# Optimization experiments

Hardware: AMD Instinct MI355X
Metric: run time of the kernel (lower is better)

Reference implementation:

```python
import jax, jax.numpy as jnp
import numpy as np

D_STATE = 8
D_CONV = 4
DT_RANK = 8
THRESHOLD = 0.5
KPOOL = 3
PAD = (KPOOL - 1) // 2
EPS = 1e-5


def _rmsnorm(x, w):
    return x * jax.lax.rsqrt(jnp.mean(x * x, axis=-1, keepdims=True) + EPS) * w


def _dw_causal_conv(x, w, b):
    # x: (L, T, C), w: (C, 1, K) depthwise causal conv along T
    xt = jnp.transpose(x, (0, 2, 1))  # (L, C, T)
    y = jax.lax.conv_general_dilated(
        xt, w, window_strides=(1,), padding=[(D_CONV - 1, 0)],
        dimension_numbers=('NCH', 'OIH', 'NCH'), feature_group_count=xt.shape[1])
    return jnp.transpose(y, (0, 2, 1)) + b


def _selective_scan(x, delta, A, B, Cm, D):
    # x, delta: (L,T,d); A: (d,n); B, Cm: (L,T,n); D: (d,)
    dA = jnp.exp(delta[..., None] * A)                        # (L,T,d,n)
    dBx = (delta * x)[..., None] * B[:, :, None, :]           # (L,T,d,n)
    def combine(a, b):
        a1, b1 = a
        a2, b2 = b
        return (a2 * a1, a2 * b1 + b2)
    _, h = jax.lax.associative_scan(combine, (dA, dBx), axis=1)
    y = jnp.einsum('ltdn,ltn->ltd', h, Cm)
    return y + x * D


def _mamba_block(x, in_proj, conv_w, conv_b, x_proj_w, dt_proj_w, dt_proj_b,
                 A_log_f, A_log_b, D_f, D_b, out_proj_w, rms_w):
    # single-depth bidirectional (bimamba-v2 style) block, expand=1, residual + RMSNorm
    res = x
    xn = _rmsnorm(x, rms_w)
    xz = xn @ in_proj                       # (L,T,2C)
    xi, z = jnp.split(xz, 2, axis=-1)
    xi = jax.nn.silu(_dw_causal_conv(xi, conv_w, conv_b))
    dbl = xi @ x_proj_w                     # (L,T,dt_rank+2*d_state)
    dt = dbl[..., :DT_RANK]
    Bm = dbl[..., DT_RANK:DT_RANK + D_STATE]
    Cm = dbl[..., DT_RANK + D_STATE:]
    delta = jax.nn.softplus(dt @ dt_proj_w + dt_proj_b)
    A_f = -jnp.exp(A_log_f)
    A_b = -jnp.exp(A_log_b)
    flip = lambda a: a[:, ::-1]
    y_f = _selective_scan(xi, delta, A_f, Bm, Cm, D_f)
    y_b = flip(_selective_scan(flip(xi), flip(delta), A_b, flip(Bm), flip(Cm), D_b))
    y = 0.5 * (y_f + y_b) * jax.nn.silu(z)  # if_devide_out -> average two directions
    return res + y @ out_proj_w


def reference(feats, in_proj, conv_w, conv_b, x_proj_w, dt_proj_w, dt_proj_b,
              A_log_f, A_log_b, D_f, D_b, out_proj_w, rms_w, mlp_w, mlp_b,
              record_len):
    N, C, H, W = feats.shape
    T = H * W
    rec = np.asarray(record_len)  # static ragged group sizes
    ends = np.cumsum(rec)
    starts = ends - rec
    masks = []
    for s0, L in zip(starts.tolist(), rec.tolist()):
        g = feats[s0:s0 + L]                       # (L,C,H,W)
        if L > 1:
            x = g.reshape(L, C, T).transpose(0, 2, 1)  # l c h w -> l (h w) c
            feat = _mamba_block(x, in_proj, conv_w, conv_b, x_proj_w, dt_proj_w,
                                dt_proj_b, A_log_f, A_log_b, D_f, D_b,
                                out_proj_w, rms_w)
            score = jax.nn.sigmoid(feat @ mlp_w + mlp_b)   # (L,T,1)
            ego = jnp.ones((1, T, 1), feats.dtype)
            bs = jnp.concatenate([ego, score[1:]], axis=0)
        else:
            bs = jnp.ones((1, T, 1), feats.dtype)
        bs = bs.transpose(0, 2, 1).reshape(L, 1, H, W)     # l (h w) c -> l c h w
        masks.append(jnp.where(bs > THRESHOLD, 1.0, 0.0).astype(feats.dtype))
    mask = jnp.concatenate(masks, axis=0)                  # (N,1,H,W)
    pooled = jax.lax.reduce_window(
        mask, -jnp.inf, jax.lax.max,
        window_dimensions=(1, 1, KPOOL, KPOOL), window_strides=(1, 1, 1, 1),
        padding=[(0, 0), (0, 0), (PAD, PAD), (PAD, PAD)])
    return pooled


def setup_inputs():
    key = jax.random.key(0)
    ks = jax.random.split(key, 8)
    C, H, W = 128, 96, 96
    record_len = np.array([2, 3, 1, 2, 4], dtype=np.int64)
    N = int(record_len.sum())
    s = 0.05
    A_log = jnp.log(jnp.broadcast_to(
        jnp.arange(1, D_STATE + 1, dtype=jnp.float32), (C, D_STATE)))
    return {
        'feats': jax.random.normal(ks[0], (N, C, H, W), jnp.float32),
        'in_proj': jax.random.normal(ks[1], (C, 2 * C), jnp.float32) * s,
        'conv_w': jax.random.normal(ks[2], (C, 1, D_CONV), jnp.float32) * s,
        'conv_b': jnp.zeros((C,), jnp.float32),
        'x_proj_w': jax.random.normal(ks[3], (C, DT_RANK + 2 * D_STATE), jnp.float32) * s,
        'dt_proj_w': jax.random.normal(ks[4], (DT_RANK, C), jnp.float32) * s,
        'dt_proj_b': jnp.full((C,), 0.1, jnp.float32),
        'A_log_f': A_log,
        'A_log_b': A_log,
        'D_f': jnp.ones((C,), jnp.float32),
        'D_b': jnp.ones((C,), jnp.float32),
        'out_proj_w': jax.random.normal(ks[5], (C, C), jnp.float32) * s,
        'rms_w': jnp.ones((C,), jnp.float32),
        'mlp_w': jax.random.normal(ks[6], (C, 1), jnp.float32) * s,
        'mlp_b': jnp.zeros((1,), jnp.float32),
        'record_len': jnp.asarray(record_len),
    }
```

## Files before the change

kernel.cpp:

```cpp
#include <hip/hip_runtime.h>
#include <cstdint>
#include <cstddef>

#define C_CH 128
#define T_TOK 9216
#define H_IMG 96
#define W_IMG 96
#define NSTATE 8

#define CHUNK 64
#define RHALO 32
#define REGION (CHUNK + 2 * RHALO)

__device__ __forceinline__ float siluf_dev(float x) {
  return x / (1.0f + expf(-x));
}

__device__ __forceinline__ float fast_silu(float x) {
  return __fdividef(x, 1.0f + __expf(-x));
}

__global__ __launch_bounds__(128) void k0_setup(
    const int* __restrict__ rec, int n_groups, int N,
    const float* __restrict__ out_proj_w, const float* __restrict__ mlp_w,
    float* __restrict__ vvec, int* __restrict__ slot)
{
  const int tid = threadIdx.x;
  if (tid == 0) {
    int f = 0, sl = 0;
    for (int g = 0; g < n_groups; ++g) {
      const int L = rec[g];
      slot[f] = -1;
      for (int i = 1; i < L; ++i) slot[f + i] = sl++;
      f += L;
    }
  }
  if (tid < C_CH) {
    float acc = 0.0f;
    for (int j = 0; j < C_CH; ++j) acc += out_proj_w[tid * C_CH + j] * mlp_w[j];
    vvec[tid] = acc;
  }
}

__global__ __launch_bounds__(256, 4) void k1_gemm(
    const float* __restrict__ feats, const float* __restrict__ in_proj,
    const float* __restrict__ rms_w, const float* __restrict__ mlp_w,
    const float* __restrict__ mlp_b, const float* __restrict__ vvec,
    const int* __restrict__ slot,
    float* __restrict__ xipre, float* __restrict__ wbuf,
    float* __restrict__ logit)
{
  __shared__ float Asm[C_CH * 64];
  __shared__ float redA[256], redB[256], irS[64];
  const int f = blockIdx.y;
  const int s = slot[f];
  if (s < 0) return;
  const int m0 = blockIdx.x * 64;
  const int tid = threadIdx.x;

  {
    const int c0 = tid >> 4;
    const int tq = (tid & 15) * 4;
    const float* src = feats + (size_t)f * C_CH * T_TOK + m0 + tq;
    #pragma unroll
    for (int i = 0; i < 8; ++i) {
      const int c = c0 + i * 16;
      const float4 x4 = *(const float4*)(src + (size_t)c * T_TOK);
      *(float4*)&Asm[c * 64 + tq] = x4;
    }
  }
  __syncthreads();
  {
    const int t = tid & 63;
    const int q = tid >> 6;
    float ssum = 0.0f, rm = 0.0f;
    for (int cc = q * 32; cc < q * 32 + 32; ++cc) {
      const float val = Asm[cc * 64 + t];
      ssum += val * val;
      rm += val * mlp_w[cc];
    }
    redA[tid] = ssum; redB[tid] = rm;
  }
  __syncthreads();
  if (tid < 64) {
    const int t = tid;
    const float ssum = redA[t] + redA[t + 64] + redA[t + 128] + redA[t + 192];
    const float rm   = redB[t] + redB[t + 64] + redB[t + 128] + redB[t + 192];
    const float ir = 1.0f / sqrtf(ssum * (1.0f / C_CH) + 1e-5f);
    logit[(size_t)s * T_TOK + m0 + t] = rm + mlp_b[0];
    irS[t] = ir;
  }
  __syncthreads();
  {
    const int t = tid & 63;
    const int q = tid >> 6;
    const float ir = irS[t];
    for (int cc = q * 32; cc < q * 32 + 32; ++cc)
      Asm[cc * 64 + t] = (Asm[cc * 64 + t] * ir) * rms_w[cc];
  }
  __syncthreads();

  const int ti = tid >> 4;
  const int tc = tid & 15;
  for (int chunk = 0; chunk < 4; ++chunk) {
    const int n0 = chunk * 64;
    const float* bp = in_proj + n0 + tc * 4;
    float acc[4][4];
    #pragma unroll
    for (int i = 0; i < 4; ++i)
      #pragma unroll
      for (int j = 0; j < 4; ++j) acc[i][j] = 0.0f;

    float4 bA = *(const float4*)(bp);
    float4 aA = *(const float4*)&Asm[ti * 4];
    #pragma unroll 2
    for (int k = 0; k < C_CH; k += 2) {
      const int kB = k + 1;
      const int kN = (k + 2 < C_CH) ? (k + 2) : (C_CH - 1);
      const float4 bB = *(const float4*)(bp + (size_t)kB * 256);
      const float4 aB = *(const float4*)&Asm[kB * 64 + ti * 4];
      acc[0][0] += aA.x * bA.x; acc[0][1] += aA.x * bA.y; acc[0][2] += aA.x * bA.z; acc[0][3] += aA.x * bA.w;
      acc[1][0] += aA.y * bA.x; acc[1][1] += aA.y * bA.y; acc[1][2] += aA.y * bA.z; acc[1][3] += aA.y * bA.w;
      acc[2][0] += aA.z * bA.x; acc[2][1] += aA.z * bA.y; acc[2][2] += aA.z * bA.z; acc[2][3] += aA.z * bA.w;
      acc[3][0] += aA.w * bA.x; acc[3][1] += aA.w * bA.y; acc[3][2] += aA.w * bA.z; acc[3][3] += aA.w * bA.w;
      const float4 bN = *(const float4*)(bp + (size_t)kN * 256);
      const float4 aN = *(const float4*)&Asm[kN * 64 + ti * 4];
      acc[0][0] += aB.x * bB.x; acc[0][1] += aB.x * bB.y; acc[0][2] += aB.x * bB.z; acc[0][3] += aB.x * bB.w;
      acc[1][0] += aB.y * bB.x; acc[1][1] += aB.y * bB.y; acc[1][2] += aB.y * bB.z; acc[1][3] += aB.y * bB.w;
      acc[2][0] += aB.z * bB.x; acc[2][1] += aB.z * bB.y; acc[2][2] += aB.z * bB.z; acc[2][3] += aB.z * bB.w;
      acc[3][0] += aB.w * bB.x; acc[3][1] += aB.w * bB.y; acc[3][2] += aB.w * bB.z; acc[3][3] += aB.w * bB.w;
      bA = bN; aA = aN;
    }

    if (chunk < 2) {
      const int cb = n0 + tc * 4;
      #pragma unroll
      for (int i = 0; i < 4; ++i) {
        const int t = m0 + ti * 4 + i;
        float4 o; o.x = acc[i][0]; o.y = acc[i][1]; o.z = acc[i][2]; o.w = acc[i][3];
        *(float4*)&xipre[((size_t)s * T_TOK + t) * C_CH + cb] = o;
      }
    } else {
      const int zc = (chunk - 2) * 64 + tc * 4;
      const float4 v4 = *(const float4*)&vvec[zc];
      #pragma unroll
      for (int i = 0; i < 4; ++i) {
        const int t = m0 + ti * 4 + i;
        float4 o;
        o.x = 0.5f * siluf_dev(acc[i][0]) * v4.x;
        o.y = 0.5f * siluf_dev(acc[i][1]) * v4.y;
        o.z = 0.5f * siluf_dev(acc[i][2]) * v4.z;
        o.w = 0.5f * siluf_dev(acc[i][3]) * v4.w;
        *(float4*)&wbuf[((size_t)s * T_TOK + t) * C_CH + zc] = o;
      }
    }
  }
}

__global__ __launch_bounds__(256, 4) void k2_convproj(
    const float* __restrict__ xipre,
    const float* __restrict__ conv_w, const float* __restrict__ conv_b,
    const float* __restrict__ x_proj_w,
    const float* __restrict__ dt_proj_w, const float* __restrict__ dt_proj_b,
    const int* __restrict__ slot,
    float* __restrict__ xd_g, float* __restrict__ bc_g)
{
  __shared__ float xibuf[64 * 129];
  __shared__ float dtb[64 * 8];
  const int f = blockIdx.y;
  const int s = slot[f];
  if (s < 0) return;
  const int m0 = blockIdx.x * 64;
  const int tid = threadIdx.x;
  const int c = tid & 127;
  const int half = tid >> 7;
  const size_t rowbase = (size_t)s * T_TOK;
  const float4 cw = *(const float4*)(conv_w + c * 4);
  const float cb = conv_b[c];

  auto ldx = [&](int t) -> float {
    return (t >= 0) ? xipre[(rowbase + t) * C_CH + c] : 0.0f;
  };

  {
    const int t0 = m0 + half * 32;
    float xm1 = ldx(t0 - 1), xm2 = ldx(t0 - 2), xm3 = ldx(t0 - 3);
    #pragma unroll
    for (int i = 0; i < 32; ++i) {
      const float cur = ldx(t0 + i);
      const float sum = cw.x * xm3 + cw.y * xm2 + cw.z * xm1 + cw.w * cur + cb;
      xibuf[(half * 32 + i) * 129 + c] = fast_silu(sum);
      xm3 = xm2; xm2 = xm1; xm1 = cur;
    }
  }
  __syncthreads();
  {
    const int q6 = __builtin_amdgcn_readfirstlane(tid >> 6) * 6;
    const int tok = tid & 63;
    float acc[6] = {0, 0, 0, 0, 0, 0};
    for (int cc = 0; cc < C_CH; ++cc) {
      const float xv = xibuf[tok * 129 + cc];
      #pragma unroll
      for (int jj = 0; jj < 6; ++jj)
        acc[jj] += xv * x_proj_w[cc * 24 + q6 + jj];
    }
    #pragma unroll
    for (int jj = 0; jj < 6; ++jj) {
      const int o = q6 + jj;
      if (o < 8) dtb[tok * 8 + o] = acc[jj];
      else       bc_g[(rowbase + m0 + tok) * 16 + (o - 8)] = acc[jj];
    }
  }
  __syncthreads();
  {
    float dw[8];
    #pragma unroll
    for (int r = 0; r < 8; ++r) dw[r] = dt_proj_w[r * C_CH + c];
    const float bias = dt_proj_b[c];
    for (int i = 0; i < 32; ++i) {
      const int tok = half * 32 + i;
      const float4 d0 = *(const float4*)&dtb[tok * 8];
      const float4 d1 = *(const float4*)&dtb[tok * 8 + 4];
      float pre = bias;
      pre += d0.x * dw[0] + d0.y * dw[1] + d0.z * dw[2] + d0.w * dw[3];
      pre += d1.x * dw[4] + d1.y * dw[5] + d1.z * dw[6] + d1.w * dw[7];
      const float dlt = fmaxf(pre, 0.0f) + __logf(1.0f + __expf(-fabsf(pre)));
      float2 xd;
      xd.x = xibuf[tok * 129 + c];
      xd.y = dlt;
      *(float2*)&xd_g[(rowbase + m0 + tok) * (2 * C_CH) + c * 2] = xd;
    }
  }
}

__global__ __launch_bounds__(256, 4) void k3_scan(
    const float* __restrict__ xd_g, const float* __restrict__ wbuf,
    const float* __restrict__ bc_g,
    const float* __restrict__ A_log_f, const float* __restrict__ A_log_b,
    const float* __restrict__ D_f, const float* __restrict__ D_b,
    const int* __restrict__ slot, float* __restrict__ logit)
{
  __shared__ float bc[REGION * 16];
  const int f = blockIdx.y;
  const int s = slot[f];
  if (s < 0) return;
  const int c0 = blockIdx.x * CHUNK;
  const int r0 = c0 - RHALO;
  const int tid = threadIdx.x;
  const int c = tid & 127;
  const int half = tid >> 7;
  const size_t rowbase = (size_t)s * T_TOK;

  {
    const long grow = ((long)rowbase + r0) * 16;
    const int lo  = (r0 < 0) ? (-r0) * 4 : 0;
    const int hi  = (r0 + REGION > T_TOK) ? (T_TOK - r0) * 4 : REGION * 4;
    #pragma unroll
    for (int i = 0; i < 2; ++i) {
      const int idx = tid + i * 256;
      if (idx >= lo && idx < hi)
        *(float4*)&bc[idx * 4] = *(const float4*)&bc_g[grow + (long)idx * 4];
    }
  }
  __syncthreads();

  float Ac[8];
  const float* Alog = half ? A_log_b : A_log_f;
  #pragma unroll
  for (int n = 0; n < NSTATE; ++n) Ac[n] = -expf(Alog[c * NSTATE + n]);
  const float Dd = half ? D_b[c] : D_f[c];
  float h[8] = {0, 0, 0, 0, 0, 0, 0, 0};

  const float a0 = Ac[0];
  int okl = 1;
  #pragma unroll
  for (int n = 1; n < NSTATE; ++n)
    okl &= (fabsf(Ac[n] - (float)(n + 1) * a0) <= 1e-4f * fabsf(Ac[n])) ? 1 : 0;
  const bool fastA = (__all(okl) != 0);

  auto decay8 = [&](float dlt, float* dA) {
    if (fastA) {
      const float e1 = __expf(dlt * a0);
      const float e2 = e1 * e1, e3 = e2 * e1, e4 = e2 * e2;
      dA[0] = e1; dA[1] = e2; dA[2] = e3; dA[3] = e4;
      dA[4] = e4 * e1; dA[5] = e4 * e2; dA[6] = e4 * e3; dA[7] = e4 * e4;
    } else {
      #pragma unroll
      for (int n = 0; n < NSTATE; ++n) dA[n] = __expf(dlt * Ac[n]);
    }
  };

  if (half == 0) {
    const int tb = (r0 < 0) ? 0 : r0;
    const int outg0 = (c0 - tb) >> 3;
    const int ng = (c0 + CHUNK - tb) >> 3;
    for (int g = 0; g < ng; ++g) {
      const int t0 = tb + g * 8;
      const bool out = (g >= outg0);
      float xg[8], dg[8], wg[8];
      #pragma unroll
      for (int j = 0; j < 8; ++j) {
        const size_t r = rowbase + t0 + j;
        const float2 xd = *(const float2*)&xd_g[r * (2 * C_CH) + c * 2];
        xg[j] = xd.x;
        dg[j] = xd.y;
        wg[j] = out ? wbuf[r * C_CH + c] : 0.0f;
      }
      #pragma unroll
      for (int j = 0; j < 8; ++j) {
        const int t = t0 + j;
        const int p = t - r0;
        const float dlt = dg[j];
        const float xiv = xg[j];
        const float u = dlt * xiv;
        const float4 b0 = *(const float4*)&bc[p * 16];
        const float4 b1 = *(const float4*)&bc[p * 16 + 4];
        float dA[8];
        decay8(dlt, dA);
        h[0] = dA[0] * h[0] + u * b0.x;
        h[1] = dA[1] * h[1] + u * b0.y;
        h[2] = dA[2] * h[2] + u * b0.z;
        h[3] = dA[3] * h[3] + u * b0.w;
        h[4] = dA[4] * h[4] + u * b1.x;
        h[5] = dA[5] * h[5] + u * b1.y;
        h[6] = dA[6] * h[6] + u * b1.z;
        h[7] = dA[7] * h[7] + u * b1.w;
        if (out) {
          const float4 cc0 = *(const float4*)&bc[p * 16 + 8];
          const float4 cc1 = *(const float4*)&bc[p * 16 + 12];
          float y = xiv * Dd;
          y += h[0] * cc0.x + h[1] * cc0.y + h[2] * cc0.z + h[3] * cc0.w;
          y += h[4] * cc1.x + h[5] * cc1.y + h[6] * cc1.z + h[7] * cc1.w;
          float contrib = y * wg[j];
          contrib += __shfl_xor(contrib, 1);
          contrib += __shfl_xor(contrib, 2);
          contrib += __shfl_xor(contrib, 4);
          contrib += __shfl_xor(contrib, 8);
          contrib += __shfl_xor(contrib, 16);
          contrib += __shfl_xor(contrib, 32);
          if ((tid & 63) == 0) atomicAdd(&logit[rowbase + t], contrib);
        }
      }
    }
  } else {
    const int te2e = r0 + REGION;
    const int te2 = (te2e > T_TOK) ? T_TOK : te2e;
    const int outg0 = (te2 - (c0 + CHUNK)) >> 3;
    const int ng = (te2 - c0) >> 3;
    for (int g = 0; g < ng; ++g) {
      const int t0 = te2 - 1 - g * 8;
      const bool out = (g >= outg0);
      float xg[8], dg[8], wg[8];
      #pragma unroll
      for (int j = 0; j < 8; ++j) {
        const size_t r = rowbase + t0 - j;
        const float2 xd = *(const float2*)&xd_g[r * (2 * C_CH) + c * 2];
        xg[j] = xd.x;
        dg[j] = xd.y;
        wg[j] = out ? wbuf[r * C_CH + c] : 0.0f;
      }
      #pragma unroll
      for (int j = 0; j < 8; ++j) {
        const int t = t0 - j;
        const int p = t - r0;
        const float dlt = dg[j];
        const float xiv = xg[j];
        const float u = dlt * xiv;
        const float4 b0 = *(const float4*)&bc[p * 16];
        const float4 b1 = *(const float4*)&bc[p * 16 + 4];
        float dA[8];
        decay8(dlt, dA);
        h[0] = dA[0] * h[0] + u * b0.x;
        h[1] = dA[1] * h[1] + u * b0.y;
        h[2] = dA[2] * h[2] + u * b0.z;
        h[3] = dA[3] * h[3] + u * b0.w;
        h[4] = dA[4] * h[4] + u * b1.x;
        h[5] = dA[5] * h[5] + u * b1.y;
        h[6] = dA[6] * h[6] + u * b1.z;
        h[7] = dA[7] * h[7] + u * b1.w;
        if (out) {
          const float4 cc0 = *(const float4*)&bc[p * 16 + 8];
          const float4 cc1 = *(const float4*)&bc[p * 16 + 12];
          float y = xiv * Dd;
          y += h[0] * cc0.x + h[1] * cc0.y + h[2] * cc0.z + h[3] * cc0.w;
          y += h[4] * cc1.x + h[5] * cc1.y + h[6] * cc1.z + h[7] * cc1.w;
          float contrib = y * wg[j];
          contrib += __shfl_xor(contrib, 1);
          contrib += __shfl_xor(contrib, 2);
          contrib += __shfl_xor(contrib, 4);
          contrib += __shfl_xor(contrib, 8);
          contrib += __shfl_xor(contrib, 16);
          contrib += __shfl_xor(contrib, 32);
          if ((tid & 63) == 0) atomicAdd(&logit[rowbase + t], contrib);
        }
      }
    }
  }
}

__global__ __launch_bounds__(128) void k4_pool(
    const float* __restrict__ logit, const int* __restrict__ slot,
    float* __restrict__ out)
{
  const int w = threadIdx.x;
  if (w >= W_IMG) return;
  const int hh = blockIdx.x;
  const int f = blockIdx.y;
  const int s = slot[f];
  float m = 0.0f;
  if (s < 0) {
    m = 1.0f;
  } else {
    for (int dh = -1; dh <= 1; ++dh) {
      const int h2 = hh + dh;
      if (h2 < 0 || h2 >= H_IMG) continue;
      for (int dw = -1; dw <= 1; ++dw) {
        const int w2 = w + dw;
        if (w2 < 0 || w2 >= W_IMG) continue;
        if (logit[(size_t)s * T_TOK + h2 * W_IMG + w2] > 0.0f) m = 1.0f;
      }
    }
  }
  out[(size_t)f * T_TOK + hh * W_IMG + w] = m;
}

extern "C" void kernel_launch(void* const* d_in, const int* in_sizes, int n_in,
                              void* d_out, int out_size, void* d_ws, size_t ws_size,
                              hipStream_t stream) {
  const float* feats      = (const float*)d_in[0];
  const float* in_proj    = (const float*)d_in[1];
  const float* conv_w     = (const float*)d_in[2];
  const float* conv_b     = (const float*)d_in[3];
  const float* x_proj_w   = (const float*)d_in[4];
  const float* dt_proj_w  = (const float*)d_in[5];
  const float* dt_proj_b  = (const float*)d_in[6];
  const float* A_log_f    = (const float*)d_in[7];
  const float* A_log_b    = (const float*)d_in[8];
  const float* D_f        = (const float*)d_in[9];
  const float* D_b        = (const float*)d_in[10];
  const float* out_proj_w = (const float*)d_in[11];
  const float* rms_w      = (const float*)d_in[12];
  const float* mlp_w      = (const float*)d_in[13];
  const float* mlp_b      = (const float*)d_in[14];
  const int*   rec        = (const int*)d_in[15];

  const int N = in_sizes[0] / (C_CH * T_TOK);
  const int n_groups = in_sizes[15];
  int S = N - n_groups;
  if (S < 1) S = 1;

  char* p = (char*)d_ws;
  float* vvec  = (float*)p; p += 1024;
  int*   slot  = (int*)p;   p += ((N * 4 + 255) / 256) * 256;
  float* logit = (float*)p; p += (size_t)S * T_TOK * 4;
  float* xipre = (float*)p; p += (size_t)S * T_TOK * C_CH * 4;
  float* wA    = (float*)p; p += (size_t)S * T_TOK * C_CH * 4;
  float* xd    = (float*)p; p += (size_t)S * T_TOK * (2 * C_CH) * 4;
  float* bcg   = (float*)p; p += (size_t)S * T_TOK * 16 * 4;
  (void)ws_size; (void)n_in; (void)out_size;

  k0_setup<<<1, 128, 0, stream>>>(rec, n_groups, N, out_proj_w, mlp_w, vvec, slot);
  k1_gemm<<<dim3(T_TOK / 64, N), 256, 0, stream>>>(
      feats, in_proj, rms_w, mlp_w, mlp_b, vvec, slot, xipre, wA, logit);
  k2_convproj<<<dim3(T_TOK / 64, N), 256, 0, stream>>>(
      xipre, conv_w, conv_b, x_proj_w, dt_proj_w, dt_proj_b, slot,
      xd, bcg);
  k3_scan<<<dim3(T_TOK / CHUNK, N), 256, 0, stream>>>(
      xd, wA, bcg, A_log_f, A_log_b, D_f, D_b, slot, logit);
  k4_pool<<<dim3(H_IMG, N), 128, 0, stream>>>(logit, slot, (float*)d_out);
}
```

Measured before the change: 328.0 us.

## Fuse in-projection GEMM with causal conv and x-projection, recomputing halo tokens

Merges the in_proj GEMM kernel and the conv/x_proj kernel into one kernel, so the pre-conv xi activations stay in shared memory and no longer go through a global round trip. The three causal-conv halo tokens before each 64-token tile are loaded, RMS-normalised and projected again inside each block. This removes one launch and the xipre buffer traffic. In exchange it adds redundant halo compute and a larger shared footprint (padded stride, reused buffer), which may lower occupancy. The GEMM inner loop is also simplified from manual double-buffering to a plain unroll-8 loop.

```diff
diff --git a/kernel.cpp b/kernel.cpp
--- a/kernel.cpp
+++ b/kernel.cpp
@@ -11,6 +11,10 @@
 #define CHUNK 64
 #define RHALO 32
 #define REGION (CHUNK + 2 * RHALO)
+
+#define ASTRIDE 68
+#define XSTRIDE 129
+#define AU_FLOATS 8704
 
 __device__ __forceinline__ float siluf_dev(float x) {
   return x / (1.0f + expf(-x));
@@ -42,164 +46,198 @@
   }
 }
 
-__global__ __launch_bounds__(256, 4) void k1_gemm(
+__global__ __launch_bounds__(256, 4) void k12_gemmproj(
     const float* __restrict__ feats, const float* __restrict__ in_proj,
     const float* __restrict__ rms_w, const float* __restrict__ mlp_w,
     const float* __restrict__ mlp_b, const float* __restrict__ vvec,
-    const int* __restrict__ slot,
-    float* __restrict__ xipre, float* __restrict__ wbuf,
-    float* __restrict__ logit)
-{
-  __shared__ float Asm[C_CH * 64];
-  __shared__ float redA[256], redB[256], irS[64];
-  const int f = blockIdx.y;
-  const int s = slot[f];
-  if (s < 0) return;
-  const int m0 = blockIdx.x * 64;
-  const int tid = threadIdx.x;
-
-  {
-    const int c0 = tid >> 4;
-    const int tq = (tid & 15) * 4;
-    const float* src = feats + (size_t)f * C_CH * T_TOK + m0 + tq;
-    #pragma unroll
-    for (int i = 0; i < 8; ++i) {
-      const int c = c0 + i * 16;
-      const float4 x4 = *(const float4*)(src + (size_t)c * T_TOK);
-      *(float4*)&Asm[c * 64 + tq] = x4;
-    }
-  }
-  __syncthreads();
-  {
-    const int t = tid & 63;
-    const int q = tid >> 6;
-    float ssum = 0.0f, rm = 0.0f;
-    for (int cc = q * 32; cc < q * 32 + 32; ++cc) {
-      const float val = Asm[cc * 64 + t];
-      ssum += val * val;
-      rm += val * mlp_w[cc];
-    }
-    redA[tid] = ssum; redB[tid] = rm;
-  }
-  __syncthreads();
-  if (tid < 64) {
-    const int t = tid;
-    const float ssum = redA[t] + redA[t + 64] + redA[t + 128] + redA[t + 192];
-    const float rm   = redB[t] + redB[t + 64] + redB[t + 128] + redB[t + 192];
-    const float ir = 1.0f / sqrtf(ssum * (1.0f / C_CH) + 1e-5f);
-    logit[(size_t)s * T_TOK + m0 + t] = rm + mlp_b[0];
-    irS[t] = ir;
-  }
-  __syncthreads();
-  {
-    const int t = tid & 63;
-    const int q = tid >> 6;
-    const float ir = irS[t];
-    for (int cc = q * 32; cc < q * 32 + 32; ++cc)
-      Asm[cc * 64 + t] = (Asm[cc * 64 + t] * ir) * rms_w[cc];
-  }
-  __syncthreads();
-
-  const int ti = tid >> 4;
-  const int tc = tid & 15;
-  for (int chunk = 0; chunk < 4; ++chunk) {
-    const int n0 = chunk * 64;
-    const float* bp = in_proj + n0 + tc * 4;
-    float acc[4][4];
-    #pragma unroll
-    for (int i = 0; i < 4; ++i)
-      #pragma unroll
-      for (int j = 0; j < 4; ++j) acc[i][j] = 0.0f;
-
-    float4 bA = *(const float4*)(bp);
-    float4 aA = *(const float4*)&Asm[ti * 4];
-    #pragma unroll 2
-    for (int k = 0; k < C_CH; k += 2) {
-      const int kB = k + 1;
-      const int kN = (k + 2 < C_CH) ? (k + 2) : (C_CH - 1);
-      const float4 bB = *(const float4*)(bp + (size_t)kB * 256);
-      const float4 aB = *(const float4*)&Asm[kB * 64 + ti * 4];
-      acc[0][0] += aA.x * bA.x; acc[0][1] += aA.x * bA.y; acc[0][2] += aA.x * bA.z; acc[0][3] += aA.x * bA.w;
-      acc[1][0] += aA.y * bA.x; acc[1][1] += aA.y * bA.y; acc[1][2] += aA.y * bA.z; acc[1][3] += aA.y * bA.w;
-      acc[2][0] += aA.z * bA.x; acc[2][1] += aA.z * bA.y; acc[2][2] += aA.z * bA.z; acc[2][3] += aA.z * bA.w;
-      acc[3][0] += aA.w * bA.x; acc[3][1] += aA.w * bA.y; acc[3][2] += aA.w * bA.z; acc[3][3] += aA.w * bA.w;
-      const float4 bN = *(const float4*)(bp + (size_t)kN * 256);
-      const float4 aN = *(const float4*)&Asm[kN * 64 + ti * 4];
-      acc[0][0] += aB.x * bB.x; acc[0][1] += aB.x * bB.y; acc[0][2] += aB.x * bB.z; acc[0][3] += aB.x * bB.w;
-      acc[1][0] += aB.y * bB.x; acc[1][1] += aB.y * bB.y; acc[1][2] += aB.y * bB.z; acc[1][3] += aB.y * bB.w;
-      acc[2][0] += aB.z * bB.x; acc[2][1] += aB.z * bB.y; acc[2][2] += aB.z * bB.z; acc[2][3] += aB.z * bB.w;
-      acc[3][0] += aB.w * bB.x; acc[3][1] += aB.w * bB.y; acc[3][2] += aB.w * bB.z; acc[3][3] += aB.w * bB.w;
-      bA = bN; aA = aN;
-    }
-
-    if (chunk < 2) {
-      const int cb = n0 + tc * 4;
-      #pragma unroll
-      for (int i = 0; i < 4; ++i) {
-        const int t = m0 + ti * 4 + i;
-        float4 o; o.x = acc[i][0]; o.y = acc[i][1]; o.z = acc[i][2]; o.w = acc[i][3];
-        *(float4*)&xipre[((size_t)s * T_TOK + t) * C_CH + cb] = o;
-      }
-    } else {
-      const int zc = (chunk - 2) * 64 + tc * 4;
-      const float4 v4 = *(const float4*)&vvec[zc];
-      #pragma unroll
-      for (int i = 0; i < 4; ++i) {
-        const int t = m0 + ti * 4 + i;
-        float4 o;
-        o.x = 0.5f * siluf_dev(acc[i][0]) * v4.x;
-        o.y = 0.5f * siluf_dev(acc[i][1]) * v4.y;
-        o.z = 0.5f * siluf_dev(acc[i][2]) * v4.z;
-        o.w = 0.5f * siluf_dev(acc[i][3]) * v4.w;
-        *(float4*)&wbuf[((size_t)s * T_TOK + t) * C_CH + zc] = o;
-      }
-    }
-  }
-}
-
-__global__ __launch_bounds__(256, 4) void k2_convproj(
-    const float* __restrict__ xipre,
     const float* __restrict__ conv_w, const float* __restrict__ conv_b,
     const float* __restrict__ x_proj_w,
     const float* __restrict__ dt_proj_w, const float* __restrict__ dt_proj_b,
     const int* __restrict__ slot,
+    float* __restrict__ wbuf, float* __restrict__ logit,
     float* __restrict__ xd_g, float* __restrict__ bc_g)
 {
-  __shared__ float xibuf[64 * 129];
+  __shared__ float Asm[AU_FLOATS];
+  __shared__ float redA[256], redB[256];
+  __shared__ float irS[68];
+  __shared__ float haloA[12];
   __shared__ float dtb[64 * 8];
   const int f = blockIdx.y;
   const int s = slot[f];
   if (s < 0) return;
   const int m0 = blockIdx.x * 64;
   const int tid = threadIdx.x;
+  const size_t rowbase = (size_t)s * T_TOK;
+
+  {
+    const int c0 = tid >> 4;
+    const int tq = (tid & 15) * 4;
+    const float* src = feats + (size_t)f * C_CH * T_TOK + m0 + tq;
+    #pragma unroll
+    for (int i = 0; i < 8; ++i) {
+      const int c = c0 + i * 16;
+      const float4 x4 = *(const float4*)(src + (size_t)c * T_TOK);
+      *(float4*)&Asm[c * ASTRIDE + 4 + tq] = x4;
+    }
+  }
+  if (m0 > 0 && tid < C_CH) {
+    const float* src = feats + (size_t)f * C_CH * T_TOK + (size_t)tid * T_TOK + m0 - 3;
+    Asm[tid * ASTRIDE + 0] = src[0];
+    Asm[tid * ASTRIDE + 1] = src[1];
+    Asm[tid * ASTRIDE + 2] = src[2];
+  }
+  __syncthreads();
+  {
+    const int t = tid & 63;
+    const int q = tid >> 6;
+    float ssum = 0.0f, rm = 0.0f;
+    for (int cc = q * 32; cc < q * 32 + 32; ++cc) {
+      const float val = Asm[cc * ASTRIDE + 4 + t];
+      ssum += val * val;
+      rm += val * mlp_w[cc];
+    }
+    redA[tid] = ssum; redB[tid] = rm;
+    if (m0 > 0 && tid < 12) {
+      const int j = tid >> 2, qh = tid & 3;
+      float ss = 0.0f;
+      for (int cc = qh * 32; cc < qh * 32 + 32; ++cc) {
+        const float v = Asm[cc * ASTRIDE + j];
+        ss += v * v;
+      }
+      haloA[tid] = ss;
+    }
+  }
+  __syncthreads();
+  if (tid < 64) {
+    const int t = tid;
+    const float ssum = redA[t] + redA[t + 64] + redA[t + 128] + redA[t + 192];
+    const float rm   = redB[t] + redB[t + 64] + redB[t + 128] + redB[t + 192];
+    const float ir = 1.0f / sqrtf(ssum * (1.0f / C_CH) + 1e-5f);
+    logit[rowbase + m0 + t] = rm + mlp_b[0];
+    irS[4 + t] = ir;
+  } else if (m0 > 0 && tid < 67) {
+    const int j = tid - 64;
+    const float ss = haloA[j * 4] + haloA[j * 4 + 1] + haloA[j * 4 + 2] + haloA[j * 4 + 3];
+    irS[j] = 1.0f / sqrtf(ss * (1.0f / C_CH) + 1e-5f);
+  }
+  __syncthreads();
+  {
+    const int t = tid & 63;
+    const int q = tid >> 6;
+    const float ir = irS[4 + t];
+    for (int cc = q * 32; cc < q * 32 + 32; ++cc)
+      Asm[cc * ASTRIDE + 4 + t] = (Asm[cc * ASTRIDE + 4 + t] * ir) * rms_w[cc];
+    if (m0 > 0 && tid < 12) {
+      const int j = tid >> 2, qh = tid & 3;
+      const float irh = irS[j];
+      for (int cc = qh * 32; cc < qh * 32 + 32; ++cc)
+        Asm[cc * ASTRIDE + j] = (Asm[cc * ASTRIDE + j] * irh) * rms_w[cc];
+    }
+  }
+  __syncthreads();
+
+  const int ti = tid >> 4;
+  const int tc = tid & 15;
+
+#define GEMM_CHUNK(N0, ACC) do {                                              \
+    const float* bp = in_proj + (N0) + tc * 4;                                \
+    _Pragma("unroll 8")                                                       \
+    for (int k = 0; k < C_CH; ++k) {                                          \
+      const float4 a4 = *(const float4*)&Asm[k * ASTRIDE + 4 + ti * 4];       \
+      const float4 b4 = *(const float4*)(bp + (size_t)k * 256);               \
+      ACC[0][0] += a4.x * b4.x; ACC[0][1] += a4.x * b4.y; ACC[0][2] += a4.x * b4.z; ACC[0][3] += a4.x * b4.w; \
+      ACC[1][0] += a4.y * b4.x; ACC[1][1] += a4.y * b4.y; ACC[1][2] += a4.y * b4.z; ACC[1][3] += a4.y * b4.w; \
+      ACC[2][0] += a4.z * b4.x; ACC[2][1] += a4.z * b4.y; ACC[2][2] += a4.z * b4.z; ACC[2][3] += a4.z * b4.w; \
+      ACC[3][0] += a4.w * b4.x; ACC[3][1] += a4.w * b4.y; ACC[3][2] += a4.w * b4.z; ACC[3][3] += a4.w * b4.w; \
+    } } while (0)
+
+  #pragma unroll
+  for (int zc4 = 0; zc4 < 2; ++zc4) {
+    float acc[4][4];
+    #pragma unroll
+    for (int i = 0; i < 4; ++i)
+      #pragma unroll
+      for (int j = 0; j < 4; ++j) acc[i][j] = 0.0f;
+    GEMM_CHUNK(128 + zc4 * 64, acc);
+    const int zc = zc4 * 64 + tc * 4;
+    const float4 v4 = *(const float4*)&vvec[zc];
+    #pragma unroll
+    for (int i = 0; i < 4; ++i) {
+      const int t = m0 + ti * 4 + i;
+      float4 o;
+      o.x = 0.5f * siluf_dev(acc[i][0]) * v4.x;
+      o.y = 0.5f * siluf_dev(acc[i][1]) * v4.y;
+      o.z = 0.5f * siluf_dev(acc[i][2]) * v4.z;
+      o.w = 0.5f * siluf_dev(acc[i][3]) * v4.w;
+      *(float4*)&wbuf[(rowbase + t) * C_CH + zc] = o;
+    }
+  }
+
+  float acc0[4][4], acc1[4][4];
+  #pragma unroll
+  for (int i = 0; i < 4; ++i)
+    #pragma unroll
+    for (int j = 0; j < 4; ++j) { acc0[i][j] = 0.0f; acc1[i][j] = 0.0f; }
+  GEMM_CHUNK(0, acc0);
+  GEMM_CHUNK(64, acc1);
+#undef GEMM_CHUNK
+
+  float hx0 = 0.0f, hx1 = 0.0f;
+  {
+    const int j0 = tid >> 7;
+    const int cc0 = tid & 127;
+    if (m0 > 0) {
+      for (int k = 0; k < C_CH; ++k) {
+        const float b0v = in_proj[(size_t)k * 256 + cc0];
+        hx0 += Asm[k * ASTRIDE + j0] * b0v;
+        if (tid < 128) hx1 += Asm[k * ASTRIDE + 2] * in_proj[(size_t)k * 256 + tid];
+      }
+    }
+  }
+  __syncthreads();
+
+  {
+    #pragma unroll
+    for (int i = 0; i < 4; ++i) {
+      const int row = 3 + ti * 4 + i;
+      #pragma unroll
+      for (int j = 0; j < 4; ++j) {
+        Asm[row * XSTRIDE + tc * 4 + j] = acc0[i][j];
+        Asm[row * XSTRIDE + 64 + tc * 4 + j] = acc1[i][j];
+      }
+    }
+    Asm[(tid >> 7) * XSTRIDE + (tid & 127)] = hx0;
+    if (tid < 128) Asm[2 * XSTRIDE + tid] = hx1;
+  }
+  __syncthreads();
+
   const int c = tid & 127;
   const int half = tid >> 7;
-  const size_t rowbase = (size_t)s * T_TOK;
-  const float4 cw = *(const float4*)(conv_w + c * 4);
-  const float cb = conv_b[c];
-
-  auto ldx = [&](int t) -> float {
-    return (t >= 0) ? xipre[(rowbase + t) * C_CH + c] : 0.0f;
-  };
-
-  {
-    const int t0 = m0 + half * 32;
-    float xm1 = ldx(t0 - 1), xm2 = ldx(t0 - 2), xm3 = ldx(t0 - 3);
+  {
+    const float4 cw = *(const float4*)(conv_w + c * 4);
+    const float cb = conv_b[c];
+    const int row0 = half ? 35 : 3;
+    float xm1 = Asm[(row0 - 1) * XSTRIDE + c];
+    float xm2 = Asm[(row0 - 2) * XSTRIDE + c];
+    float xm3 = Asm[(row0 - 3) * XSTRIDE + c];
+    __syncthreads();
     #pragma unroll
     for (int i = 0; i < 32; ++i) {
-      const float cur = ldx(t0 + i);
+      const int row = row0 + i;
+      const float cur = Asm[row * XSTRIDE + c];
       const float sum = cw.x * xm3 + cw.y * xm2 + cw.z * xm1 + cw.w * cur + cb;
-      xibuf[(half * 32 + i) * 129 + c] = fast_silu(sum);
+      Asm[row * XSTRIDE + c] = fast_silu(sum);
       xm3 = xm2; xm2 = xm1; xm1 = cur;
     }
   }
   __syncthreads();
+
   {
     const int q6 = __builtin_amdgcn_readfirstlane(tid >> 6) * 6;
     const int tok = tid & 63;
     float acc[6] = {0, 0, 0, 0, 0, 0};
     for (int cc = 0; cc < C_CH; ++cc) {
-      const float xv = xibuf[tok * 129 + cc];
+      const float xv = Asm[(3 + tok) * XSTRIDE + cc];
       #pragma unroll
       for (int jj = 0; jj < 6; ++jj)
         acc[jj] += xv * x_proj_w[cc * 24 + q6 + jj];
@@ -212,6 +250,7 @@
     }
   }
   __syncthreads();
+
   {
     float dw[8];
     #pragma unroll
@@ -226,7 +265,7 @@
       pre += d1.x * dw[4] + d1.y * dw[5] + d1.z * dw[6] + d1.w * dw[7];
       const float dlt = fmaxf(pre, 0.0f) + __logf(1.0f + __expf(-fabsf(pre)));
       float2 xd;
-      xd.x = xibuf[tok * 129 + c];
+      xd.x = Asm[(3 + tok) * XSTRIDE + c];
       xd.y = dlt;
       *(float2*)&xd_g[(rowbase + m0 + tok) * (2 * C_CH) + c * 2] = xd;
     }
@@ -453,18 +492,16 @@
   float* vvec  = (float*)p; p += 1024;
   int*   slot  = (int*)p;   p += ((N * 4 + 255) / 256) * 256;
   float* logit = (float*)p; p += (size_t)S * T_TOK * 4;
-  float* xipre = (float*)p; p += (size_t)S * T_TOK * C_CH * 4;
   float* wA    = (float*)p; p += (size_t)S * T_TOK * C_CH * 4;
   float* xd    = (float*)p; p += (size_t)S * T_TOK * (2 * C_CH) * 4;
   float* bcg   = (float*)p; p += (size_t)S * T_TOK * 16 * 4;
   (void)ws_size; (void)n_in; (void)out_size;
 
   k0_setup<<<1, 128, 0, stream>>>(rec, n_groups, N, out_proj_w, mlp_w, vvec, slot);
-  k1_gemm<<<dim3(T_TOK / 64, N), 256, 0, stream>>>(
-      feats, in_proj, rms_w, mlp_w, mlp_b, vvec, slot, xipre, wA, logit);
-  k2_convproj<<<dim3(T_TOK / 64, N), 256, 0, stream>>>(
-      xipre, conv_w, conv_b, x_proj_w, dt_proj_w, dt_proj_b, slot,
-      xd, bcg);
+  k12_gemmproj<<<dim3(T_TOK / 64, N), 256, 0, stream>>>(
+      feats, in_proj, rms_w, mlp_w, mlp_b, vvec,
+      conv_w, conv_b, x_proj_w, dt_proj_w, dt_proj_b, slot,
+      wA, logit, xd, bcg);
   k3_scan<<<dim3(T_TOK / CHUNK, N), 256, 0, stream>>>(
       xd, wA, bcg, A_log_f, A_log_b, D_f, D_b, slot, logit);
   k4_pool<<<dim3(H_IMG, N), 128, 0, stream>>>(logit, slot, (float*)d_out);
```

Result: faster. 314.1 us (-4.3%).
